# Kernel tuning notes

Measured on AMD Instinct MI355X. Metric: run time of the kernel, lower is better.

The kernel has to match this reference:

```python
import jax, jax.numpy as jnp
import numpy as np

D_MODEL = 512
NUM_HEADS = 8


def setup_inputs() -> dict:
    key = jax.random.key(0)
    ks = jax.random.split(key, 12)
    B, S, D = 2, 4096, D_MODEL
    s = 1.0 / np.sqrt(D)
    return {
        "q": jax.random.normal(ks[0], (B, S, D), jnp.float32),
        "k": jax.random.normal(ks[1], (B, S, D), jnp.float32),
        "v": jax.random.normal(ks[2], (B, S, D), jnp.float32),
        "w_q": jax.random.normal(ks[3], (D, D), jnp.float32) * s,
        "b_q": jax.random.normal(ks[4], (D,), jnp.float32) * s,
        "w_k": jax.random.normal(ks[5], (D, D), jnp.float32) * s,
        "b_k": jax.random.normal(ks[6], (D,), jnp.float32) * s,
        "w_v": jax.random.normal(ks[7], (D, D), jnp.float32) * s,
        "b_v": jax.random.normal(ks[8], (D,), jnp.float32) * s,
        "w_o": jax.random.normal(ks[9], (D, D), jnp.float32) * s,
        "b_o": jax.random.normal(ks[10], (D,), jnp.float32) * s,
    }


def _split(x, num_heads):
    B, S, D = x.shape
    return x.reshape(B, S, num_heads, D // num_heads).transpose(0, 2, 1, 3)


def reference(q, k, v, w_q, b_q, w_k, b_k, w_v, b_v, w_o, b_o):
    # Linear projections (torch Linear: x @ W^T + b)
    qp = q @ w_q.T + b_q
    kp = k @ w_k.T + b_k
    vp = v @ w_v.T + b_v
    # split into heads: [B, H, S, d_head]
    qh = _split(qp, NUM_HEADS)
    kh = _split(kp, NUM_HEADS)
    vh = _split(vp, NUM_HEADS)
    d_head = qh.shape[-1]
    # NOTE: original scales by sqrt(d_model of the per-head tensor) == sqrt(d_head)
    score = jnp.einsum("bhqd,bhkd->bhqk", qh, kh) / jnp.sqrt(jnp.float32(d_head))
    attn = jax.nn.softmax(score, axis=-1)  # full [B,H,S,S] materialized, as in source
    out = jnp.einsum("bhqk,bhkd->bhqd", attn, vh)
    # concat heads back to [B, S, D]
    B, H, S, Dh = out.shape
    out = out.transpose(0, 2, 1, 3).reshape(B, S, H * Dh)
    return out @ w_o.T + b_o
```

## Files before the change

kernel.cpp:

```cpp
#include <hip/hip_runtime.h>
#include <math.h>

typedef __bf16 bf16_t;
typedef __bf16 bf16x4_v __attribute__((ext_vector_type(4)));
typedef __bf16 bf16x8_t __attribute__((ext_vector_type(8)));
typedef float f32x4_t __attribute__((ext_vector_type(4)));
typedef short short4_t __attribute__((ext_vector_type(4)));
typedef unsigned uint2_t __attribute__((ext_vector_type(2)));

#define S_LEN 4096
#define DM 512
#define NH 8
#define DH 64
#define MTOT 8192

#define Q_SCALE 0.1803368801111204f

#define REG   4194304
#define WREG  262144
#define W_OFF (3 * REG)
#define CVT_TOTAL (3 * REG + 4 * WREG)
#define QH_OFF CVT_TOTAL

__device__ inline f32x4_t mfma16(bf16x8_t a, bf16x8_t b, f32x4_t c) {
    return __builtin_amdgcn_mfma_f32_16x16x32_bf16(a, b, c, 0, 0, 0);
}

__device__ inline f32x4_t mfma_pv(short4_t a, short4_t b, f32x4_t c) {
    return __builtin_amdgcn_mfma_f32_16x16x16bf16_1k(a, b, c, 0, 0, 0);
}

__device__ inline unsigned pkbf16(float a, float b) {
    unsigned short ra = __builtin_bit_cast(unsigned short, (bf16_t)a);
    unsigned short rb = __builtin_bit_cast(unsigned short, (bf16_t)b);
    return (unsigned)ra | ((unsigned)rb << 16);
}

__device__ inline void async_copy16(const void* g, void* l) {
    __builtin_amdgcn_global_load_lds(
        (const __attribute__((address_space(1))) void*)g,
        (__attribute__((address_space(3))) void*)l, 16, 0, 0);
}

__global__ __launch_bounds__(256) void cvt_all(
    const float* __restrict__ q, const float* __restrict__ k, const float* __restrict__ v,
    const float* __restrict__ wq, const float* __restrict__ wk,
    const float* __restrict__ wv, const float* __restrict__ wo,
    bf16_t* __restrict__ dst)
{
    long gidx = (long)blockIdx.x * 2048 + (long)threadIdx.x * 8;
    const float* src;
    long off = gidx;
    if      (gidx < 1L * REG)          { src = q; }
    else if (gidx < 2L * REG)          { src = k;  off = gidx - 1L * REG; }
    else if (gidx < 3L * REG)          { src = v;  off = gidx - 2L * REG; }
    else if (gidx < W_OFF + 1L * WREG) { src = wq; off = gidx - W_OFF; }
    else if (gidx < W_OFF + 2L * WREG) { src = wk; off = gidx - (W_OFF + 1L * WREG); }
    else if (gidx < W_OFF + 3L * WREG) { src = wv; off = gidx - (W_OFF + 2L * WREG); }
    else                               { src = wo; off = gidx - (W_OFF + 3L * WREG); }
    float4 a = *(const float4*)(src + off);
    float4 b = *(const float4*)(src + off + 4);
    bf16x8_t h;
    h[0] = (bf16_t)a.x; h[1] = (bf16_t)a.y; h[2] = (bf16_t)a.z; h[3] = (bf16_t)a.w;
    h[4] = (bf16_t)b.x; h[5] = (bf16_t)b.y; h[6] = (bf16_t)b.z; h[7] = (bf16_t)b.w;
    *(bf16x8_t*)(dst + gidx) = h;
}

__global__ __launch_bounds__(256) void gemm_qkv(
    const bf16_t* __restrict__ XWb,
    const float* __restrict__ B0, const float* __restrict__ B1, const float* __restrict__ B2,
    bf16_t* __restrict__ dst_base)
{
    const int p = blockIdx.z;
    const bf16_t* __restrict__ X = XWb + (size_t)p * REG;
    const bf16_t* __restrict__ W = XWb + W_OFF + (size_t)p * WREG;
    const float* __restrict__ Bi = (p == 0) ? B0 : ((p == 1) ? B1 : B2);
    bf16_t* __restrict__ dst = dst_base + (size_t)p * REG;

    const int m0 = blockIdx.x * 128;
    const int n0 = blockIdx.y * 128;
    const int tid = threadIdx.x;
    const int lane = tid & 63, wid = tid >> 6;
    const int lm = lane & 15, lg = lane >> 4;
    const int wm = (wid >> 1) * 64, wn = (wid & 1) * 64;

    __shared__ __align__(16) bf16_t As[128 * 64];
    __shared__ __align__(16) bf16_t Bs[128 * 64];

    f32x4_t acc[4][4] = {};

    const int r0 = tid >> 3, c7 = tid & 7;
    const int cA0 = ((lg) ^ (lm & 7)) * 8;
    const int cA1 = ((4 + lg) ^ (lm & 7)) * 8;

    for (int kb = 0; kb < DM / 64; ++kb) {
        const int k0 = kb * 64;
#pragma unroll
        for (int i = 0; i < 4; ++i) {
            int row = i * 32 + r0;
            int ch = c7 ^ (row & 7);
            async_copy16(X + (size_t)(m0 + row) * DM + k0 + ch * 8, (char*)As + (i * 256 + tid) * 16);
            async_copy16(W + (size_t)(n0 + row) * DM + k0 + ch * 8, (char*)Bs + (i * 256 + tid) * 16);
        }
        __syncthreads();
#pragma unroll
        for (int kd = 0; kd < 2; ++kd) {
            const int co = kd ? cA1 : cA0;
            bf16x8_t fa[4], fb[4];
#pragma unroll
            for (int mt = 0; mt < 4; ++mt) {
                fa[mt] = *(const bf16x8_t*)(As + (wm + mt * 16 + lm) * 64 + co);
                fb[mt] = *(const bf16x8_t*)(Bs + (wn + mt * 16 + lm) * 64 + co);
            }
            if (p < 2) {
#pragma unroll
                for (int mt = 0; mt < 4; ++mt)
#pragma unroll
                    for (int nt = 0; nt < 4; ++nt)
                        acc[nt][mt] = mfma16(fb[nt], fa[mt], acc[nt][mt]);
            } else {
#pragma unroll
                for (int mt = 0; mt < 4; ++mt)
#pragma unroll
                    for (int nt = 0; nt < 4; ++nt)
                        acc[mt][nt] = mfma16(fa[mt], fb[nt], acc[mt][nt]);
            }
        }
        __syncthreads();
    }

    if (p == 2) {
#pragma unroll
        for (int nt = 0; nt < 4; ++nt) {
            int col = n0 + wn + nt * 16 + lm;
            float bv = Bi[col];
            int h = (col >> 6) & 7, dc = col & 63;
#pragma unroll
            for (int mt = 0; mt < 4; ++mt) {
                int mrow = m0 + wm + mt * 16 + lg * 4;
                int bb = mrow >> 12, s = mrow & (S_LEN - 1);
                bf16x4_v pk;
#pragma unroll
                for (int r = 0; r < 4; ++r) pk[r] = (bf16_t)(acc[mt][nt][r] + bv);
                *(bf16x4_v*)&dst[(((size_t)(bb * NH + h)) * DH + dc) * S_LEN + s] = pk;
            }
        }
    } else {
        const float scale = (p == 0) ? Q_SCALE : 1.0f;
#pragma unroll
        for (int nt = 0; nt < 4; ++nt) {
            int ncol = n0 + wn + nt * 16 + lg * 4;
            float4 bv4 = *(const float4*)&Bi[ncol];
            int h = (ncol >> 6) & 7, dc = ncol & 63;
#pragma unroll
            for (int mt = 0; mt < 4; ++mt) {
                int m = m0 + wm + mt * 16 + lm;
                int bb = m >> 12, s = m & (S_LEN - 1);
                bf16x4_v pk;
                pk[0] = (bf16_t)((acc[nt][mt][0] + bv4.x) * scale);
                pk[1] = (bf16_t)((acc[nt][mt][1] + bv4.y) * scale);
                pk[2] = (bf16_t)((acc[nt][mt][2] + bv4.z) * scale);
                pk[3] = (bf16_t)((acc[nt][mt][3] + bv4.w) * scale);
                *(bf16x4_v*)&dst[(((size_t)(bb * NH + h)) * S_LEN + s) * DH + dc] = pk;
            }
        }
    }
}

__global__ __launch_bounds__(512, 4) void flash_attn(
    const bf16_t* __restrict__ Qh, const bf16_t* __restrict__ Kh,
    const bf16_t* __restrict__ Vth, bf16_t* __restrict__ O)
{
    const int bh = blockIdx.y;
    const int q0 = blockIdx.x * 128;
    const int tid = threadIdx.x;
    const int lane = tid & 63, wid = tid >> 6;
    const int lm = lane & 15, lg = lane >> 4;
    const int qg = wid & 3;
    const int kvh = wid >> 2;

    const bf16_t* __restrict__ Qb  = Qh  + (size_t)bh * S_LEN * DH;
    const bf16_t* __restrict__ Kb  = Kh  + (size_t)bh * S_LEN * DH;
    const bf16_t* __restrict__ Vtg = Vth + (size_t)bh * S_LEN * DH;

    __shared__ __align__(16) char smem[35328];

    bf16x8_t bQ[2][2];
#pragma unroll
    for (int nt = 0; nt < 2; ++nt)
#pragma unroll
        for (int kd = 0; kd < 2; ++kd)
            bQ[nt][kd] = *(const bf16x8_t*)(Qb + (size_t)(q0 + qg * 32 + nt * 16 + lm) * DH + kd * 32 + lg * 8);

    f32x4_t o_acc[4][2] = {};
    float l_acc[2] = {0.f, 0.f};

    const int srow = tid >> 3;
    const int slch = (tid & 7) ^ (srow & 7);
    char* lK0 = smem + tid * 16;
    char* lK1 = smem + 8192 + tid * 16;
    char* lV0 = smem + 16384 + tid * 16;
    char* lV1 = smem + 24576 + tid * 16;
    const bf16_t* gK = Kb + (size_t)srow * DH + slch * 8;
    const bf16_t* gV = Vtg + (size_t)srow * S_LEN + slch * 8;

    const int cK0 = ((lg) ^ (lm & 7)) * 16;
    const int cK1 = ((4 + lg) ^ (lm & 7)) * 16;
    const char* ksb = smem + kvh * 8192;
    const char* vsb = smem + 16384 + kvh * 8192;

    for (int it = 0; it < S_LEN / 128; ++it) {
        const int kvb = it * 128;
        async_copy16(gK + (size_t)kvb * DH, lK0);
        async_copy16(gK + (size_t)(kvb + 64) * DH, lK1);
        async_copy16(gV + kvb, lV0);
        async_copy16(gV + kvb + 64, lV1);
        __syncthreads();

        unsigned pk[4][2][2];
#pragma unroll
        for (int mt = 0; mt < 4; ++mt) {
            const char* krow = ksb + (mt * 16 + lm) * 128;
            bf16x8_t aK0 = *(const bf16x8_t*)(krow + cK0);
            bf16x8_t aK1 = *(const bf16x8_t*)(krow + cK1);
            f32x4_t s0 = {}, s1 = {};
            s0 = mfma16(aK0, bQ[0][0], s0);
            s0 = mfma16(aK1, bQ[0][1], s0);
            s1 = mfma16(aK0, bQ[1][0], s1);
            s1 = mfma16(aK1, bQ[1][1], s1);
            float e0 = __builtin_amdgcn_exp2f(s0[0]);
            float e1 = __builtin_amdgcn_exp2f(s0[1]);
            float e2 = __builtin_amdgcn_exp2f(s0[2]);
            float e3 = __builtin_amdgcn_exp2f(s0[3]);
            pk[mt][0][0] = pkbf16(e0, e1);
            pk[mt][0][1] = pkbf16(e2, e3);
            l_acc[0] += (e0 + e1) + (e2 + e3);
            float f0 = __builtin_amdgcn_exp2f(s1[0]);
            float f1 = __builtin_amdgcn_exp2f(s1[1]);
            float f2 = __builtin_amdgcn_exp2f(s1[2]);
            float f3 = __builtin_amdgcn_exp2f(s1[3]);
            pk[mt][1][0] = pkbf16(f0, f1);
            pk[mt][1][1] = pkbf16(f2, f3);
            l_acc[1] += (f0 + f1) + (f2 + f3);
        }

#pragma unroll
        for (int mt = 0; mt < 4; ++mt) {
            const char* vrow = vsb + (mt * 16 + lm) * 128;
#pragma unroll
            for (int c = 0; c < 4; ++c) {
                int pc = (c * 2 + (lg >> 1)) ^ (lm & 7);
                short4_t vA = *(const short4_t*)(vrow + pc * 16 + (lg & 1) * 8);
                short4_t bP0 = __builtin_bit_cast(short4_t, (uint2_t){pk[c][0][0], pk[c][0][1]});
                short4_t bP1 = __builtin_bit_cast(short4_t, (uint2_t){pk[c][1][0], pk[c][1][1]});
                o_acc[mt][0] = mfma_pv(vA, bP0, o_acc[mt][0]);
                o_acc[mt][1] = mfma_pv(vA, bP1, o_acc[mt][1]);
            }
        }
        __syncthreads();
    }

#pragma unroll
    for (int nt = 0; nt < 2; ++nt) {
        l_acc[nt] += __shfl_xor(l_acc[nt], 16, 64);
        l_acc[nt] += __shfl_xor(l_acc[nt], 32, 64);
    }

    float* ob = (float*)smem + qg * (32 * 66);
    float* lb = (float*)(smem + 33792);

    if (kvh == 1) {
#pragma unroll
        for (int nt = 0; nt < 2; ++nt) {
#pragma unroll
            for (int mt = 0; mt < 4; ++mt)
#pragma unroll
                for (int r = 0; r < 4; ++r)
                    ob[(nt * 16 + lm) * 66 + mt * 16 + lg * 4 + r] = o_acc[mt][nt][r];
            if (lg == 0) lb[qg * 32 + nt * 16 + lm] = l_acc[nt];
        }
    }
    __syncthreads();
    if (kvh == 0) {
        const int bb = bh >> 3, h = bh & 7;
#pragma unroll
        for (int nt = 0; nt < 2; ++nt) {
            float ltot = l_acc[nt] + lb[qg * 32 + nt * 16 + lm];
            float inv = 1.0f / ltot;
            int q = q0 + qg * 32 + nt * 16 + lm;
            size_t base = ((size_t)(bb * S_LEN + q)) * DM + h * DH;
#pragma unroll
            for (int mt = 0; mt < 4; ++mt) {
                const float* orow = &ob[(nt * 16 + lm) * 66 + mt * 16 + lg * 4];
                bf16x4_v pkd;
#pragma unroll
                for (int r = 0; r < 4; ++r)
                    pkd[r] = (bf16_t)((o_acc[mt][nt][r] + orow[r]) * inv);
                *(bf16x4_v*)&O[base + mt * 16 + lg * 4] = pkd;
            }
        }
    }
}

__global__ __launch_bounds__(256) void gemm_out(
    const bf16_t* __restrict__ A, const bf16_t* __restrict__ W,
    const float* __restrict__ Bi, float* __restrict__ out)
{
    const int m0 = blockIdx.x * 64;
    const int n0 = blockIdx.y * 128;
    const int tid = threadIdx.x;
    const int lane = tid & 63, wid = tid >> 6;
    const int lm = lane & 15, lg = lane >> 4;
    const int wm = (wid >> 1) * 32, wn = (wid & 1) * 64;

    __shared__ __align__(16) bf16_t As[64 * 64];
    __shared__ __align__(16) bf16_t Bs[128 * 64];

    f32x4_t acc[4][2] = {};

    const int r0 = tid >> 3, c7 = tid & 7;
    const int cA0 = ((lg) ^ (lm & 7)) * 8;
    const int cA1 = ((4 + lg) ^ (lm & 7)) * 8;

    for (int kb = 0; kb < DM / 64; ++kb) {
        const int k0 = kb * 64;
#pragma unroll
        for (int i = 0; i < 2; ++i) {
            int idx = i * 256 + tid;
            int row = idx >> 3;
            int ch = (idx & 7) ^ (row & 7);
            async_copy16(A + (size_t)(m0 + row) * DM + k0 + ch * 8, (char*)As + idx * 16);
        }
#pragma unroll
        for (int i = 0; i < 4; ++i) {
            int row = i * 32 + r0;
            int ch = c7 ^ (row & 7);
            async_copy16(W + (size_t)(n0 + row) * DM + k0 + ch * 8, (char*)Bs + (i * 256 + tid) * 16);
        }
        __syncthreads();
#pragma unroll
        for (int kd = 0; kd < 2; ++kd) {
            const int co = kd ? cA1 : cA0;
            bf16x8_t fa[2], fb[4];
#pragma unroll
            for (int mt = 0; mt < 2; ++mt)
                fa[mt] = *(const bf16x8_t*)(As + (wm + mt * 16 + lm) * 64 + co);
#pragma unroll
            for (int nt = 0; nt < 4; ++nt)
                fb[nt] = *(const bf16x8_t*)(Bs + (wn + nt * 16 + lm) * 64 + co);
#pragma unroll
            for (int nt = 0; nt < 4; ++nt)
#pragma unroll
                for (int mt = 0; mt < 2; ++mt)
                    acc[nt][mt] = mfma16(fb[nt], fa[mt], acc[nt][mt]);
        }
        __syncthreads();
    }

#pragma unroll
    for (int nt = 0; nt < 4; ++nt) {
        int ncol = n0 + wn + nt * 16 + lg * 4;
        float4 bv4 = *(const float4*)&Bi[ncol];
#pragma unroll
        for (int mt = 0; mt < 2; ++mt) {
            int m = m0 + wm + mt * 16 + lm;
            float4 ov;
            ov.x = acc[nt][mt][0] + bv4.x;
            ov.y = acc[nt][mt][1] + bv4.y;
            ov.z = acc[nt][mt][2] + bv4.z;
            ov.w = acc[nt][mt][3] + bv4.w;
            *(float4*)&out[(size_t)m * DM + ncol] = ov;
        }
    }
}

extern "C" void kernel_launch(void* const* d_in, const int* in_sizes, int n_in,
                              void* d_out, int out_size, void* d_ws, size_t ws_size,
                              hipStream_t stream)
{
    const float* q  = (const float*)d_in[0];
    const float* k  = (const float*)d_in[1];
    const float* v  = (const float*)d_in[2];
    const float* wq = (const float*)d_in[3];
    const float* bq = (const float*)d_in[4];
    const float* wk = (const float*)d_in[5];
    const float* bk = (const float*)d_in[6];
    const float* wv = (const float*)d_in[7];
    const float* bv = (const float*)d_in[8];
    const float* wo = (const float*)d_in[9];
    const float* bo = (const float*)d_in[10];
    float* out = (float*)d_out;

    bf16_t* ws = (bf16_t*)d_ws;
    bf16_t* XWb = ws;
    bf16_t* Qh  = ws + QH_OFF;
    bf16_t* Kh  = Qh + REG;
    bf16_t* VTh = Kh + REG;
    bf16_t* Ob  = ws;
    bf16_t* Wob = ws + W_OFF + 3 * (size_t)WREG;

    cvt_all<<<CVT_TOTAL / 2048, 256, 0, stream>>>(q, k, v, wq, wk, wv, wo, XWb);

    dim3 g1(MTOT / 128, DM / 128, 3);
    gemm_qkv<<<g1, 256, 0, stream>>>(XWb, bq, bk, bv, Qh);

    dim3 g2(S_LEN / 128, 2 * NH, 1);
    flash_attn<<<g2, 512, 0, stream>>>(Qh, Kh, VTh, Ob);

    dim3 g3(MTOT / 64, DM / 128, 1);
    gemm_out<<<g3, 256, 0, stream>>>(Ob, Wob, bo, out);
}
```

Measured before the change: 234.9 us.

## Double-buffer K/V tiles in LDS and use 16x16x32 MFMA for PV

Adds a two-stage LDS ping-pong buffer so the next K/V tile's async global-to-LDS copy is issued before computing on the current tile, dropping one barrier per iteration. The PV product switches from 16x16x16 MFMA to 16x16x32 MFMA by packing two K-chunks per instruction, halving the PV MFMA count. LDS use grows from about 35 KB to 64 KB per block, which can lower occupancy below the 4-blocks launch bound. The single barrier per iteration still protects buffer reuse, since a buffer is refilled only after the next barrier.

Result: faster. 227.6 us (-3.1%).

```diff
diff --git a/kernel.cpp b/kernel.cpp
--- a/kernel.cpp
+++ b/kernel.cpp
@@ -5,8 +5,8 @@
 typedef __bf16 bf16x4_v __attribute__((ext_vector_type(4)));
 typedef __bf16 bf16x8_t __attribute__((ext_vector_type(8)));
 typedef float f32x4_t __attribute__((ext_vector_type(4)));
-typedef short short4_t __attribute__((ext_vector_type(4)));
 typedef unsigned uint2_t __attribute__((ext_vector_type(2)));
+typedef unsigned uint4_t __attribute__((ext_vector_type(4)));
 
 #define S_LEN 4096
 #define DM 512
@@ -24,10 +24,6 @@
 
 __device__ inline f32x4_t mfma16(bf16x8_t a, bf16x8_t b, f32x4_t c) {
     return __builtin_amdgcn_mfma_f32_16x16x32_bf16(a, b, c, 0, 0, 0);
-}
-
-__device__ inline f32x4_t mfma_pv(short4_t a, short4_t b, f32x4_t c) {
-    return __builtin_amdgcn_mfma_f32_16x16x16bf16_1k(a, b, c, 0, 0, 0);
 }
 
 __device__ inline unsigned pkbf16(float a, float b) {
@@ -183,7 +179,7 @@
     const bf16_t* __restrict__ Kb  = Kh  + (size_t)bh * S_LEN * DH;
     const bf16_t* __restrict__ Vtg = Vth + (size_t)bh * S_LEN * DH;
 
-    __shared__ __align__(16) char smem[35328];
+    __shared__ __align__(16) char smem[65536];
 
     bf16x8_t bQ[2][2];
 #pragma unroll
@@ -197,25 +193,36 @@
 
     const int srow = tid >> 3;
     const int slch = (tid & 7) ^ (srow & 7);
-    char* lK0 = smem + tid * 16;
-    char* lK1 = smem + 8192 + tid * 16;
-    char* lV0 = smem + 16384 + tid * 16;
-    char* lV1 = smem + 24576 + tid * 16;
     const bf16_t* gK = Kb + (size_t)srow * DH + slch * 8;
     const bf16_t* gV = Vtg + (size_t)srow * S_LEN + slch * 8;
 
     const int cK0 = ((lg) ^ (lm & 7)) * 16;
     const int cK1 = ((4 + lg) ^ (lm & 7)) * 16;
-    const char* ksb = smem + kvh * 8192;
-    const char* vsb = smem + 16384 + kvh * 8192;
-
-    for (int it = 0; it < S_LEN / 128; ++it) {
-        const int kvb = it * 128;
-        async_copy16(gK + (size_t)kvb * DH, lK0);
-        async_copy16(gK + (size_t)(kvb + 64) * DH, lK1);
-        async_copy16(gV + kvb, lV0);
-        async_copy16(gV + kvb + 64, lV1);
+
+    {
+        char* b = smem;
+        async_copy16(gK, b + tid * 16);
+        async_copy16(gK + (size_t)64 * DH, b + 8192 + tid * 16);
+        async_copy16(gV, b + 16384 + tid * 16);
+        async_copy16(gV + 64, b + 24576 + tid * 16);
+    }
+
+    const int NT = S_LEN / 128;
+    for (int it = 0; it < NT; ++it) {
+        const char* buf = smem + (it & 1) * 32768;
         __syncthreads();
+
+        if (it + 1 < NT) {
+            char* nb = smem + ((it + 1) & 1) * 32768;
+            const int kvb = (it + 1) * 128;
+            async_copy16(gK + (size_t)kvb * DH, nb + tid * 16);
+            async_copy16(gK + (size_t)(kvb + 64) * DH, nb + 8192 + tid * 16);
+            async_copy16(gV + kvb, nb + 16384 + tid * 16);
+            async_copy16(gV + kvb + 64, nb + 24576 + tid * 16);
+        }
+
+        const char* ksb = buf + kvh * 8192;
+        const char* vsb = buf + 16384 + kvh * 8192;
 
         unsigned pk[4][2][2];
 #pragma unroll
@@ -248,16 +255,19 @@
         for (int mt = 0; mt < 4; ++mt) {
             const char* vrow = vsb + (mt * 16 + lm) * 128;
 #pragma unroll
-            for (int c = 0; c < 4; ++c) {
-                int pc = (c * 2 + (lg >> 1)) ^ (lm & 7);
-                short4_t vA = *(const short4_t*)(vrow + pc * 16 + (lg & 1) * 8);
-                short4_t bP0 = __builtin_bit_cast(short4_t, (uint2_t){pk[c][0][0], pk[c][0][1]});
-                short4_t bP1 = __builtin_bit_cast(short4_t, (uint2_t){pk[c][1][0], pk[c][1][1]});
-                o_acc[mt][0] = mfma_pv(vA, bP0, o_acc[mt][0]);
-                o_acc[mt][1] = mfma_pv(vA, bP1, o_acc[mt][1]);
-            }
-        }
-        __syncthreads();
+            for (int cc = 0; cc < 2; ++cc) {
+                const int ca = 2 * cc, cb = 2 * cc + 1;
+                int pc0 = (ca * 2 + (lg >> 1)) ^ (lm & 7);
+                int pc1 = (cb * 2 + (lg >> 1)) ^ (lm & 7);
+                uint2_t va0 = *(const uint2_t*)(vrow + pc0 * 16 + (lg & 1) * 8);
+                uint2_t va1 = *(const uint2_t*)(vrow + pc1 * 16 + (lg & 1) * 8);
+                bf16x8_t vA = __builtin_bit_cast(bf16x8_t, (uint4_t){va0[0], va0[1], va1[0], va1[1]});
+                bf16x8_t bP0 = __builtin_bit_cast(bf16x8_t, (uint4_t){pk[ca][0][0], pk[ca][0][1], pk[cb][0][0], pk[cb][0][1]});
+                bf16x8_t bP1 = __builtin_bit_cast(bf16x8_t, (uint4_t){pk[ca][1][0], pk[ca][1][1], pk[cb][1][0], pk[cb][1][1]});
+                o_acc[mt][0] = mfma16(vA, bP0, o_acc[mt][0]);
+                o_acc[mt][1] = mfma16(vA, bP1, o_acc[mt][1]);
+            }
+        }
     }
 
 #pragma unroll
@@ -265,6 +275,8 @@
         l_acc[nt] += __shfl_xor(l_acc[nt], 16, 64);
         l_acc[nt] += __shfl_xor(l_acc[nt], 32, 64);
     }
+
+    __syncthreads();
 
     float* ob = (float*)smem + qg * (32 * 66);
     float* lb = (float*)(smem + 33792);
```
